# Optimization experiments

Measured on AMD Instinct MI355X. Metric: run time of the kernel, lower is better.

The kernel has to match this reference:

```python
import jax, jax.numpy as jnp
import numpy as np

B, L, D, H = 4, 2048, 1024, 16
DK = D // H  # 64


def setup_inputs() -> dict:
    key = jax.random.key(0)
    ks = jax.random.split(key, 8)
    s = 0.05
    return {
        "query": jax.random.normal(ks[0], (B, L, D), jnp.float32),
        "key": jax.random.normal(ks[1], (B, L, D), jnp.float32),
        "value": jax.random.normal(ks[2], (B, L, D), jnp.float32),
        "mask": jnp.ones((B, L, L), jnp.int32),
        "Wq": jax.random.normal(ks[3], (D, DK), jnp.float32) * s,
        "Wk": jax.random.normal(ks[4], (D, DK), jnp.float32) * s,
        "Wv": jax.random.normal(ks[5], (D, DK), jnp.float32) * s,
        "Wo": jax.random.normal(ks[6], (H * DK, D), jnp.float32) * s,
    }


def reference(query, key, value, mask, Wq, Wk, Wv, Wo):
    # Single-head projections (the torch module projects once, then reuses
    # the SAME q/k/v for every head, producing num_heads identical outputs).
    q = jnp.einsum("bld,dk->blk", query, Wq)   # [B, L, DK]
    k = jnp.einsum("bld,dk->blk", key, Wk)
    v = jnp.einsum("bld,dk->blk", value, Wv)
    scale = 1.0 / jnp.sqrt(jnp.asarray(DK, q.dtype))
    scores = jnp.einsum("bqk,bsk->bqs", q, k) * scale  # [B, L, L]
    scores = jnp.where(mask == 0, -jnp.inf, scores)
    p = jax.nn.softmax(scores, axis=-1)
    head = jnp.einsum("bqs,bsk->bqk", p, v)    # [B, L, DK]
    # Concatenation of H identical heads == tile along last dim.
    out = jnp.tile(head, (1, 1, H))             # [B, L, H*DK]
    return jnp.einsum("blh,hd->bld", out, Wo)
```

## Files before the change

### kernel.cpp

```cpp
#include <hip/hip_runtime.h>
#include <hip/hip_bf16.h>

#define Bb 4
#define Ll 2048
#define Dd 1024
#define DKk 64
#define BL (Bb*Ll)
#define G_SPLIT 8

typedef __attribute__((ext_vector_type(4))) float f32x4;
typedef __attribute__((ext_vector_type(8))) short bf16x8;

__device__ __forceinline__ unsigned short f2bf(float x) {
  unsigned int u = __builtin_bit_cast(unsigned int, x);
  u += 0x7fffu + ((u >> 16) & 1u);
  return (unsigned short)(u >> 16);
}
__device__ __forceinline__ unsigned int pack2bf(float a, float b) {
  return (unsigned int)f2bf(a) | ((unsigned int)f2bf(b) << 16);
}

__global__ __launch_bounds__(256)
void prep_kernel(const float* __restrict__ Wq, const float* __restrict__ Wk,
                 const float* __restrict__ Wv, const float* __restrict__ Wo,
                 unsigned short* __restrict__ Wfq, unsigned short* __restrict__ Wfk,
                 unsigned short* __restrict__ Wfv, unsigned short* __restrict__ WoSumT) {
  int idx = blockIdx.x * 256 + threadIdx.x;
  if (idx < 3 * 65536) {
    int which = idx >> 16;
    int r = idx & 65535;
    int n = r & 63, k = r >> 6;
    const float* W = which == 0 ? Wq : (which == 1 ? Wk : Wv);
    unsigned short* Wf = which == 0 ? Wfq : (which == 1 ? Wfk : Wfv);
    const int t = n >> 4, lr = n & 15;
    const int ks = k >> 5, g = (k >> 3) & 3, e = k & 7;
    Wf[(size_t)(((ks * 4 + t) * 4 + g) * 128) + lr * 8 + e] = f2bf(W[(size_t)k * 64 + n]);
  } else {
    int r = idx - 3 * 65536;
    int d = r & 1023, k = r >> 10;
    float s = 0.f;
#pragma unroll
    for (int h = 0; h < 16; ++h) s += Wo[(size_t)(h * 64 + k) * 1024 + d];
    WoSumT[(size_t)d * 64 + k] = f2bf(s);
  }
}

__global__ __launch_bounds__(256)
void proj_kernel(const float* __restrict__ query, const float* __restrict__ key,
                 const float* __restrict__ value,
                 const unsigned short* __restrict__ Wfq, const unsigned short* __restrict__ Wfk,
                 const unsigned short* __restrict__ Wfv,
                 unsigned short* __restrict__ Qp, unsigned short* __restrict__ Kf,
                 unsigned short* __restrict__ Vf) {
  const int which = blockIdx.y;
  const float* X = which == 0 ? query : (which == 1 ? key : value);
  const unsigned short* Wf = which == 0 ? Wfq : (which == 1 ? Wfk : Wfv);
  const int R0 = blockIdx.x * 16;

  __shared__ __align__(16) unsigned short Xl[16 * 1032];

  const int tid = threadIdx.x, w = tid >> 6, lane = tid & 63;
  const int g = lane >> 4, lr = lane & 15;

#pragma unroll
  for (int i = 0; i < 8; ++i) {
    int c = tid + 256 * i;
    int row = c >> 7, kc = c & 127;
    const float* src = X + (size_t)(R0 + row) * 1024 + kc * 8;
    f32x4 a = *(const f32x4*)src;
    f32x4 b2 = *(const f32x4*)(src + 4);
    uint4 p;
    p.x = pack2bf(a[0], a[1]);
    p.y = pack2bf(a[2], a[3]);
    p.z = pack2bf(b2[0], b2[1]);
    p.w = pack2bf(b2[2], b2[3]);
    *(uint4*)&Xl[row * 1032 + kc * 8] = p;
  }
  __syncthreads();

  f32x4 acc = (f32x4){0.f, 0.f, 0.f, 0.f};
  const unsigned short* xrow = &Xl[lr * 1032 + g * 8];
  const unsigned short* wfb = Wf + (size_t)(w * 4 + g) * 128 + lr * 8;
#pragma unroll
  for (int ks = 0; ks < 32; ++ks) {
    bf16x8 a = *(const bf16x8*)(xrow + ks * 32);
    bf16x8 b = *(const bf16x8*)(wfb + (size_t)ks * 2048);
    acc = __builtin_amdgcn_mfma_f32_16x16x32_bf16(a, b, acc, 0, 0, 0);
  }

  const int dk = w * 16 + lr;
  if (which == 0) {
#pragma unroll
    for (int i = 0; i < 4; ++i)
      Qp[(size_t)(R0 + 4 * g + i) * 64 + dk] = f2bf(acc[i]);
  } else if (which == 1) {
#pragma unroll
    for (int i = 0; i < 4; ++i) {
      const int sg = R0 + 4 * g + i;
      const int b = sg >> 11, sl = sg & 2047;
      const int tile = b * 32 + (sl >> 6), c = (sl >> 4) & 3, lrk = sl & 15;
      Kf[(size_t)tile * 4096 + (c * 8 + (dk >> 3)) * 128 + lrk * 8 + (dk & 7)] = f2bf(acc[i]);
    }
  } else {
#pragma unroll
    for (int i = 0; i < 4; ++i) {
      const int sg = R0 + 4 * g + i;
      const int b = sg >> 11, sl = sg & 2047;
      const int tile = b * 32 + (sl >> 6);
      const int h = (sl >> 5) & 1, g2 = (sl >> 3) & 3, e2 = sl & 7;
      Vf[(size_t)tile * 4096 + ((w * 2 + h) * 4 + g2) * 128 + lr * 8 + e2] = f2bf(acc[i]);
    }
  }
}

__global__ __launch_bounds__(256)
void maskpack_kernel(const int* __restrict__ mask, unsigned long long* __restrict__ BM) {
  const int wid = (blockIdx.x * 256 + threadIdx.x) >> 6;
  const int lane = threadIdx.x & 63;
  const int nw = (gridDim.x * 256) >> 6;
  for (int task = wid; task < BL * 8; task += nw) {
    const int4 m = *(const int4*)(mask + (size_t)task * 256 + lane * 4);
    unsigned long long b0 = __ballot(m.x != 0);
    unsigned long long b1 = __ballot(m.y != 0);
    unsigned long long b2 = __ballot(m.z != 0);
    unsigned long long b3 = __ballot(m.w != 0);
    unsigned long long v = lane == 0 ? b0 : lane == 1 ? b1 : lane == 2 ? b2 : b3;
    if (lane < 4) BM[(size_t)task * 4 + lane] = v;
  }
}

__global__ __launch_bounds__(128, 4)
void attn_kernel(const unsigned short* __restrict__ Qp, const unsigned short* __restrict__ Kf,
                 const unsigned short* __restrict__ Vf, const unsigned long long* __restrict__ BM,
                 float* __restrict__ Opart, float* __restrict__ lpart) {
  const int q0 = blockIdx.x * 32;
  const int gy = blockIdx.y;
  const int b = q0 >> 11;
  const int tid = threadIdx.x, lane = tid & 63, w = tid >> 6;
  const int g = lane >> 4, lr = lane & 15;

  const unsigned short* qrow = Qp + (size_t)(q0 + w * 16 + lr) * 64;
  bf16x8 qf0 = *(const bf16x8*)(qrow + g * 8);
  bf16x8 qf1 = *(const bf16x8*)(qrow + 32 + g * 8);

  const unsigned long long* bm = BM + ((size_t)(q0 + w * 16 + lr) * 8 + gy) * 4;
  const unsigned long long W0 = bm[0], W1 = bm[1], W2 = bm[2], W3 = bm[3];

  f32x4 o[4];
#pragma unroll
  for (int t = 0; t < 4; ++t) o[t] = (f32x4){0.f, 0.f, 0.f, 0.f};
  float lsum = 0.f;

  const unsigned short* Kt = Kf + (size_t)(b * 32 + gy * 4) * 4096;
  const unsigned short* Vt = Vf + (size_t)(b * 32 + gy * 4) * 4096;

#pragma unroll
  for (int st = 0; st < 4; ++st) {
    const unsigned short* Kts = Kt + st * 4096;
    const unsigned short* Vts = Vt + st * 4096;

    bf16x8 kf0[4], kf1[4];
#pragma unroll
    for (int c = 0; c < 4; ++c) {
      kf0[c] = *(const bf16x8*)(Kts + (c * 8 + g) * 128 + lr * 8);
      kf1[c] = *(const bf16x8*)(Kts + (c * 8 + 4 + g) * 128 + lr * 8);
    }

    uint2 packs[4];
#pragma unroll
    for (int c = 0; c < 4; ++c) {
      f32x4 a4 = (f32x4){0.f, 0.f, 0.f, 0.f};
      a4 = __builtin_amdgcn_mfma_f32_16x16x32_bf16(kf0[c], qf0, a4, 0, 0, 0);
      a4 = __builtin_amdgcn_mfma_f32_16x16x32_bf16(kf1[c], qf1, a4, 0, 0, 0);
      const int j = st * 16 + 4 * c + g;
      float p0 = ((W0 >> j) & 1) ? __expf(a4[0] * 0.125f) : 0.f;
      float p1 = ((W1 >> j) & 1) ? __expf(a4[1] * 0.125f) : 0.f;
      float p2 = ((W2 >> j) & 1) ? __expf(a4[2] * 0.125f) : 0.f;
      float p3 = ((W3 >> j) & 1) ? __expf(a4[3] * 0.125f) : 0.f;
      lsum += (p0 + p1) + (p2 + p3);
      packs[c].x = pack2bf(p0, p1);
      packs[c].y = pack2bf(p2, p3);
    }

#pragma unroll
    for (int h = 0; h < 2; ++h) {
      const int srcLo = lr + ((g & 1) << 5);
      const int srcHi = srcLo + 16;
      uint2 pl0 = packs[2 * h], pl1 = packs[2 * h + 1];
      unsigned a0x = __shfl((int)pl0.x, srcLo), a0y = __shfl((int)pl0.y, srcLo);
      unsigned a1x = __shfl((int)pl1.x, srcLo), a1y = __shfl((int)pl1.y, srcLo);
      unsigned b0x = __shfl((int)pl0.x, srcHi), b0y = __shfl((int)pl0.y, srcHi);
      unsigned b1x = __shfl((int)pl1.x, srcHi), b1y = __shfl((int)pl1.y, srcHi);
      const bool hisel = ((g >> 1) & 1) != 0;
      uint4 bb;
      bb.x = hisel ? a1x : a0x;
      bb.y = hisel ? a1y : a0y;
      bb.z = hisel ? b1x : b0x;
      bb.w = hisel ? b1y : b0y;
      bf16x8 pb = __builtin_bit_cast(bf16x8, bb);
#pragma unroll
      for (int t = 0; t < 4; ++t) {
        bf16x8 av = *(const bf16x8*)(Vts + ((t * 2 + h) * 4 + g) * 128 + lr * 8);
        o[t] = __builtin_amdgcn_mfma_f32_16x16x32_bf16(av, pb, o[t], 0, 0, 0);
      }
    }
  }

  lsum += __shfl_xor(lsum, 16);
  lsum += __shfl_xor(lsum, 32);

  float* Ob = Opart + ((size_t)gy * BL + q0 + w * 16 + lr) * 64;
#pragma unroll
  for (int t = 0; t < 4; ++t)
    *(f32x4*)(Ob + t * 16 + g * 4) = o[t];
  if (lane < 16)
    lpart[(size_t)gy * BL + q0 + w * 16 + lane] = lsum;
}

__global__ __launch_bounds__(256)
void combine_kernel(const float* __restrict__ Opart, const float* __restrict__ lpart,
                    unsigned short* __restrict__ Hp) {
  int idx = blockIdx.x * 256 + threadIdx.x;
  int q = idx >> 4, c0 = (idx & 15) * 4;
  float l = 0.f;
#pragma unroll
  for (int gg = 0; gg < G_SPLIT; ++gg) l += lpart[(size_t)gg * BL + q];
  float inv = 1.f / l;
  f32x4 s = (f32x4){0.f, 0.f, 0.f, 0.f};
#pragma unroll
  for (int gg = 0; gg < G_SPLIT; ++gg) {
    f32x4 a = *(const f32x4*)(Opart + ((size_t)gg * BL + q) * 64 + c0);
    s[0] += a[0]; s[1] += a[1]; s[2] += a[2]; s[3] += a[3];
  }
  uint2 pv;
  pv.x = pack2bf(s[0] * inv, s[1] * inv);
  pv.y = pack2bf(s[2] * inv, s[3] * inv);
  *(uint2*)(Hp + (size_t)q * 64 + c0) = pv;
}

__global__ __launch_bounds__(256)
void oproj_kernel(const unsigned short* __restrict__ Hp,
                  const unsigned short* __restrict__ WoSumT, float* __restrict__ out) {
  const int R0 = blockIdx.x * 64;
  const int n0 = blockIdx.y * 256;
  __shared__ __align__(16) unsigned short Hl[64 * 72];
  __shared__ __align__(16) unsigned short Wl[256 * 72];
  const int tid = threadIdx.x, lane = tid & 63, w = tid >> 6;
  const int g = lane >> 4, lr = lane & 15;

#pragma unroll
  for (int i = 0; i < 2; ++i) {
    int c = tid + 256 * i;
    int row = c >> 3, cc = c & 7;
    *(uint4*)&Hl[row * 72 + cc * 8] = *(const uint4*)(Hp + (size_t)(R0 + row) * 64 + cc * 8);
  }
#pragma unroll
  for (int i = 0; i < 8; ++i) {
    int c = tid + 256 * i;
    int row = c >> 3, cc = c & 7;
    *(uint4*)&Wl[row * 72 + cc * 8] = *(const uint4*)(WoSumT + (size_t)(n0 + row) * 64 + cc * 8);
  }
  __syncthreads();

  f32x4 acc[16];
#pragma unroll
  for (int t = 0; t < 16; ++t) acc[t] = (f32x4){0.f, 0.f, 0.f, 0.f};
#pragma unroll
  for (int kh = 0; kh < 2; ++kh) {
    bf16x8 a = *(const bf16x8*)&Hl[(w * 16 + lr) * 72 + kh * 32 + g * 8];
#pragma unroll
    for (int t = 0; t < 16; ++t) {
      bf16x8 bb = *(const bf16x8*)&Wl[(t * 16 + lr) * 72 + kh * 32 + g * 8];
      acc[t] = __builtin_amdgcn_mfma_f32_16x16x32_bf16(a, bb, acc[t], 0, 0, 0);
    }
  }
  float* ob = out + (size_t)(R0 + w * 16 + g * 4) * 1024 + n0 + lr;
#pragma unroll
  for (int t = 0; t < 16; ++t)
#pragma unroll
    for (int i = 0; i < 4; ++i)
      ob[(size_t)i * 1024 + t * 16] = acc[t][i];
}

extern "C" void kernel_launch(void* const* d_in, const int* in_sizes, int n_in,
                              void* d_out, int out_size, void* d_ws, size_t ws_size,
                              hipStream_t stream) {
  const float* query = (const float*)d_in[0];
  const float* key   = (const float*)d_in[1];
  const float* value = (const float*)d_in[2];
  const int*   mask  = (const int*)d_in[3];
  const float* Wq    = (const float*)d_in[4];
  const float* Wk    = (const float*)d_in[5];
  const float* Wv    = (const float*)d_in[6];
  const float* Wo    = (const float*)d_in[7];
  float* out = (float*)d_out;

  unsigned short* Qp   = (unsigned short*)d_ws;
  unsigned short* Kf   = Qp + (size_t)BL * 64;
  unsigned short* Vf   = Kf + (size_t)BL * 64;
  unsigned short* Wfq  = Vf + (size_t)BL * 64;
  unsigned short* Wfk  = Wfq + 65536;
  unsigned short* Wfv  = Wfk + 65536;
  unsigned short* WoSumT = Wfv + 65536;
  float* lpart = (float*)(WoSumT + 65536);
  float* Opart = lpart + (size_t)G_SPLIT * BL;
  unsigned long long* BM = (unsigned long long*)(Opart + (size_t)G_SPLIT * BL * 64);
  unsigned short* Hp = Qp;

  hipLaunchKernelGGL(prep_kernel, dim3(1024), dim3(256), 0, stream,
                     Wq, Wk, Wv, Wo, Wfq, Wfk, Wfv, WoSumT);
  hipLaunchKernelGGL(proj_kernel, dim3(512, 3), dim3(256), 0, stream,
                     query, key, value, Wfq, Wfk, Wfv, Qp, Kf, Vf);
  hipLaunchKernelGGL(maskpack_kernel, dim3(2048), dim3(256), 0, stream,
                     mask, BM);
  hipLaunchKernelGGL(attn_kernel, dim3(BL / 32, G_SPLIT), dim3(128), 0, stream,
                     Qp, Kf, Vf, BM, Opart, lpart);
  hipLaunchKernelGGL(combine_kernel, dim3(BL * 16 / 256), dim3(256), 0, stream,
                     Opart, lpart, Hp);
  hipLaunchKernelGGL(oproj_kernel, dim3(128, 4), dim3(256), 0, stream,
                     Hp, WoSumT, out);
}
```

Baseline: 74.64 us.

## Fuse mask bit-packing into attention and stream projection inputs via global_load_lds

Removes the separate maskpack kernel: each attention block now reads its own slice of the int mask and ballots it into per-row bitmasks directly, so the packed mask buffer and one launch go away. The projection kernel is restructured to load fp32 input chunks straight into LDS with global_load_lds in four K-chunks, convert to bf16 when building MFMA operands, and have each wave compute all 64 output columns for its rows. This cuts a kernel launch and intermediate traffic. In exchange it adds extra syncs and more LDS conversion work per MFMA in the projection.

```diff
diff --git a/kernel.cpp b/kernel.cpp
--- a/kernel.cpp
+++ b/kernel.cpp
@@ -10,6 +10,9 @@
 
 typedef __attribute__((ext_vector_type(4))) float f32x4;
 typedef __attribute__((ext_vector_type(8))) short bf16x8;
+
+typedef __attribute__((address_space(1))) const void gas_void;
+typedef __attribute__((address_space(3))) void las_void;
 
 __device__ __forceinline__ unsigned short f2bf(float x) {
   unsigned int u = __builtin_bit_cast(unsigned int, x);
@@ -57,81 +60,76 @@
   const unsigned short* Wf = which == 0 ? Wfq : (which == 1 ? Wfk : Wfv);
   const int R0 = blockIdx.x * 16;
 
-  __shared__ __align__(16) unsigned short Xl[16 * 1032];
+  __shared__ __align__(16) float Xl[16 * 260];
 
   const int tid = threadIdx.x, w = tid >> 6, lane = tid & 63;
   const int g = lane >> 4, lr = lane & 15;
 
-#pragma unroll
-  for (int i = 0; i < 8; ++i) {
-    int c = tid + 256 * i;
-    int row = c >> 7, kc = c & 127;
-    const float* src = X + (size_t)(R0 + row) * 1024 + kc * 8;
-    f32x4 a = *(const f32x4*)src;
-    f32x4 b2 = *(const f32x4*)(src + 4);
-    uint4 p;
-    p.x = pack2bf(a[0], a[1]);
-    p.y = pack2bf(a[2], a[3]);
-    p.z = pack2bf(b2[0], b2[1]);
-    p.w = pack2bf(b2[2], b2[3]);
-    *(uint4*)&Xl[row * 1032 + kc * 8] = p;
-  }
-  __syncthreads();
-
-  f32x4 acc = (f32x4){0.f, 0.f, 0.f, 0.f};
-  const unsigned short* xrow = &Xl[lr * 1032 + g * 8];
-  const unsigned short* wfb = Wf + (size_t)(w * 4 + g) * 128 + lr * 8;
-#pragma unroll
-  for (int ks = 0; ks < 32; ++ks) {
-    bf16x8 a = *(const bf16x8*)(xrow + ks * 32);
-    bf16x8 b = *(const bf16x8*)(wfb + (size_t)ks * 2048);
-    acc = __builtin_amdgcn_mfma_f32_16x16x32_bf16(a, b, acc, 0, 0, 0);
-  }
-
-  const int dk = w * 16 + lr;
-  if (which == 0) {
-#pragma unroll
-    for (int i = 0; i < 4; ++i)
-      Qp[(size_t)(R0 + 4 * g + i) * 64 + dk] = f2bf(acc[i]);
-  } else if (which == 1) {
-#pragma unroll
-    for (int i = 0; i < 4; ++i) {
-      const int sg = R0 + 4 * g + i;
-      const int b = sg >> 11, sl = sg & 2047;
-      const int tile = b * 32 + (sl >> 6), c = (sl >> 4) & 3, lrk = sl & 15;
-      Kf[(size_t)tile * 4096 + (c * 8 + (dk >> 3)) * 128 + lrk * 8 + (dk & 7)] = f2bf(acc[i]);
-    }
-  } else {
-#pragma unroll
-    for (int i = 0; i < 4; ++i) {
-      const int sg = R0 + 4 * g + i;
-      const int b = sg >> 11, sl = sg & 2047;
-      const int tile = b * 32 + (sl >> 6);
-      const int h = (sl >> 5) & 1, g2 = (sl >> 3) & 3, e2 = sl & 7;
-      Vf[(size_t)tile * 4096 + ((w * 2 + h) * 4 + g2) * 128 + lr * 8 + e2] = f2bf(acc[i]);
-    }
-  }
-}
-
-__global__ __launch_bounds__(256)
-void maskpack_kernel(const int* __restrict__ mask, unsigned long long* __restrict__ BM) {
-  const int wid = (blockIdx.x * 256 + threadIdx.x) >> 6;
-  const int lane = threadIdx.x & 63;
-  const int nw = (gridDim.x * 256) >> 6;
-  for (int task = wid; task < BL * 8; task += nw) {
-    const int4 m = *(const int4*)(mask + (size_t)task * 256 + lane * 4);
-    unsigned long long b0 = __ballot(m.x != 0);
-    unsigned long long b1 = __ballot(m.y != 0);
-    unsigned long long b2 = __ballot(m.z != 0);
-    unsigned long long b3 = __ballot(m.w != 0);
-    unsigned long long v = lane == 0 ? b0 : lane == 1 ? b1 : lane == 2 ? b2 : b3;
-    if (lane < 4) BM[(size_t)task * 4 + lane] = v;
+  f32x4 acc[4];
+#pragma unroll
+  for (int t = 0; t < 4; ++t) acc[t] = (f32x4){0.f, 0.f, 0.f, 0.f};
+
+  for (int cc = 0; cc < 4; ++cc) {
+    if (cc) __syncthreads();
+#pragma unroll
+    for (int j = 0; j < 4; ++j) {
+      const int row = w * 4 + j;
+      const float* gp = X + (size_t)(R0 + row) * 1024 + cc * 256 + lane * 4;
+      __builtin_amdgcn_global_load_lds((gas_void*)gp, (las_void*)&Xl[row * 260], 16, 0, 0);
+    }
+    __syncthreads();
+
+#pragma unroll
+    for (int ks = 0; ks < 8; ++ks) {
+      const float* xp = &Xl[lr * 260 + ks * 32 + g * 8];
+      f32x4 va = *(const f32x4*)xp;
+      f32x4 vb = *(const f32x4*)(xp + 4);
+      uint4 ap;
+      ap.x = pack2bf(va[0], va[1]);
+      ap.y = pack2bf(va[2], va[3]);
+      ap.z = pack2bf(vb[0], vb[1]);
+      ap.w = pack2bf(vb[2], vb[3]);
+      bf16x8 af = __builtin_bit_cast(bf16x8, ap);
+      const int kidx = cc * 8 + ks;
+#pragma unroll
+      for (int t = 0; t < 4; ++t) {
+        bf16x8 bb = *(const bf16x8*)(Wf + (size_t)((kidx * 4 + t) * 4 + g) * 128 + lr * 8);
+        acc[t] = __builtin_amdgcn_mfma_f32_16x16x32_bf16(af, bb, acc[t], 0, 0, 0);
+      }
+    }
+  }
+
+#pragma unroll
+  for (int t = 0; t < 4; ++t) {
+    const int dk = t * 16 + lr;
+    if (which == 0) {
+#pragma unroll
+      for (int i = 0; i < 4; ++i)
+        Qp[(size_t)(R0 + 4 * g + i) * 64 + dk] = f2bf(acc[t][i]);
+    } else if (which == 1) {
+#pragma unroll
+      for (int i = 0; i < 4; ++i) {
+        const int sg = R0 + 4 * g + i;
+        const int b = sg >> 11, sl = sg & 2047;
+        const int tile = b * 32 + (sl >> 6), c = (sl >> 4) & 3, lrk = sl & 15;
+        Kf[(size_t)tile * 4096 + (c * 8 + (dk >> 3)) * 128 + lrk * 8 + (dk & 7)] = f2bf(acc[t][i]);
+      }
+    } else {
+#pragma unroll
+      for (int i = 0; i < 4; ++i) {
+        const int sg = R0 + 4 * g + i;
+        const int b = sg >> 11, sl = sg & 2047;
+        const int tile = b * 32 + (sl >> 6);
+        const int h = (sl >> 5) & 1, g2 = (sl >> 3) & 3, e2 = sl & 7;
+        Vf[(size_t)tile * 4096 + ((t * 2 + h) * 4 + g2) * 128 + lr * 8 + e2] = f2bf(acc[t][i]);
+      }
+    }
   }
 }
 
 __global__ __launch_bounds__(128, 4)
 void attn_kernel(const unsigned short* __restrict__ Qp, const unsigned short* __restrict__ Kf,
-                 const unsigned short* __restrict__ Vf, const unsigned long long* __restrict__ BM,
+                 const unsigned short* __restrict__ Vf, const int* __restrict__ mask,
                  float* __restrict__ Opart, float* __restrict__ lpart) {
   const int q0 = blockIdx.x * 32;
   const int gy = blockIdx.y;
@@ -143,8 +141,30 @@
   bf16x8 qf0 = *(const bf16x8*)(qrow + g * 8);
   bf16x8 qf1 = *(const bf16x8*)(qrow + 32 + g * 8);
 
-  const unsigned long long* bm = BM + ((size_t)(q0 + w * 16 + lr) * 8 + gy) * 4;
-  const unsigned long long W0 = bm[0], W1 = bm[1], W2 = bm[2], W3 = bm[3];
+  unsigned long long W0 = 0, W1 = 0, W2 = 0, W3 = 0;
+  {
+    const int* mbase = mask + (size_t)(q0 + w * 16) * Ll + gy * 256 + lane * 4;
+#pragma unroll
+    for (int rb = 0; rb < 4; ++rb) {
+      int4 m0 = *(const int4*)(mbase + (size_t)(rb * 4 + 0) * Ll);
+      int4 m1 = *(const int4*)(mbase + (size_t)(rb * 4 + 1) * Ll);
+      int4 m2 = *(const int4*)(mbase + (size_t)(rb * 4 + 2) * Ll);
+      int4 m3 = *(const int4*)(mbase + (size_t)(rb * 4 + 3) * Ll);
+#pragma unroll
+      for (int j = 0; j < 4; ++j) {
+        int4 m = j == 0 ? m0 : (j == 1 ? m1 : (j == 2 ? m2 : m3));
+        unsigned long long c0 = __ballot(m.x != 0);
+        unsigned long long c1 = __ballot(m.y != 0);
+        unsigned long long c2 = __ballot(m.z != 0);
+        unsigned long long c3 = __ballot(m.w != 0);
+        const bool keep = (lr == rb * 4 + j);
+        W0 = keep ? c0 : W0;
+        W1 = keep ? c1 : W1;
+        W2 = keep ? c2 : W2;
+        W3 = keep ? c3 : W3;
+      }
+    }
+  }
 
   f32x4 o[4];
 #pragma unroll
@@ -304,17 +324,14 @@
   unsigned short* WoSumT = Wfv + 65536;
   float* lpart = (float*)(WoSumT + 65536);
   float* Opart = lpart + (size_t)G_SPLIT * BL;
-  unsigned long long* BM = (unsigned long long*)(Opart + (size_t)G_SPLIT * BL * 64);
   unsigned short* Hp = Qp;
 
   hipLaunchKernelGGL(prep_kernel, dim3(1024), dim3(256), 0, stream,
                      Wq, Wk, Wv, Wo, Wfq, Wfk, Wfv, WoSumT);
   hipLaunchKernelGGL(proj_kernel, dim3(512, 3), dim3(256), 0, stream,
                      query, key, value, Wfq, Wfk, Wfv, Qp, Kf, Vf);
-  hipLaunchKernelGGL(maskpack_kernel, dim3(2048), dim3(256), 0, stream,
-                     mask, BM);
   hipLaunchKernelGGL(attn_kernel, dim3(BL / 32, G_SPLIT), dim3(128), 0, stream,
-                     Qp, Kf, Vf, BM, Opart, lpart);
+                     Qp, Kf, Vf, mask, Opart, lpart);
   hipLaunchKernelGGL(combine_kernel, dim3(BL * 16 / 256), dim3(256), 0, stream,
                      Opart, lpart, Hp);
   hipLaunchKernelGGL(oproj_kernel, dim3(128, 4), dim3(256), 0, stream,
```

Result: slower. 89.27 us (+19.6%).
